# Performance work log

Measured on AMD Instinct MI355X. Metric: run time of the kernel, lower is better.

The kernel has to match this reference:

```python
import jax, jax.numpy as jnp
import numpy as np

D = 256      # d_model
H = 8        # num heads
HD = D // H  # head dim
DFF = 1024   # feedforward dim
S = 1024     # seq len
B = 8        # batch
EPS = 1e-5


def _layernorm(x, g, b):
    mu = jnp.mean(x, axis=-1, keepdims=True)
    var = jnp.mean((x - mu) ** 2, axis=-1, keepdims=True)
    return (x - mu) * jax.lax.rsqrt(var + EPS) * g + b


def setup_inputs() -> dict:
    key = jax.random.key(0)
    ks = jax.random.split(key, 12)
    xav = lambda k, shape: jax.random.uniform(
        k, shape, jnp.float32, -1.0, 1.0) * np.sqrt(6.0 / (shape[0] + shape[-1]))
    return {
        "src": jax.random.normal(ks[0], (S, B, D), jnp.float32),
        "bias": jax.random.normal(ks[1], (B, H, S, S), jnp.float32),
        "in_proj_w": xav(ks[2], (3 * D, D)),
        "in_proj_b": jnp.zeros((3 * D,), jnp.float32),
        "out_w": xav(ks[3], (D, D)),
        "out_b": jnp.zeros((D,), jnp.float32),
        "w1": xav(ks[4], (DFF, D)),
        "b1": jnp.zeros((DFF,), jnp.float32),
        "w2": xav(ks[5], (D, DFF)),
        "b2": jnp.zeros((D,), jnp.float32),
        "g1": jnp.ones((D,), jnp.float32),
        "be1": jnp.zeros((D,), jnp.float32),
        "g2": jnp.ones((D,), jnp.float32),
        "be2": jnp.zeros((D,), jnp.float32),
    }


def reference(src, bias, in_proj_w, in_proj_b, out_w, out_b,
              w1, b1, w2, b2, g1, be1, g2, be2):
    # Pre-norm (note: residual uses the NORMED src, matching the torch code)
    x = _layernorm(src, g1, be1)                       # [S,B,D]
    qkv = x @ in_proj_w.T + in_proj_b                  # [S,B,3D]
    q, k, v = jnp.split(qkv, 3, axis=-1)
    q = q * (HD ** -0.5)
    # [S,B,D] -> [B,H,S,HD]
    to_heads = lambda t: t.reshape(S, B, H, HD).transpose(1, 2, 0, 3)
    qh, kh, vh = to_heads(q), to_heads(k), to_heads(v)
    scores = jnp.einsum('bhsd,bhtd->bhst', qh, kh) + bias
    attn = jax.nn.softmax(scores, axis=-1)             # [B,H,S,S]
    ctx = jnp.einsum('bhst,bhtd->bhsd', attn, vh)      # [B,H,S,HD]
    ctx = ctx.transpose(2, 0, 1, 3).reshape(S, B, D)
    attn_out = ctx @ out_w.T + out_b
    x = x + attn_out                                   # residual (eval: no dropout)
    y = _layernorm(x, g2, be2)
    ff = jax.nn.relu(y @ w1.T + b1) @ w2.T + b2
    return y + ff
```

## Files before the change

### kernel.cpp

```cpp
#include <hip/hip_runtime.h>
#include <hip/hip_bf16.h>
#include <cstdint>

typedef unsigned short u16;
typedef __attribute__((ext_vector_type(8))) short bf16x8;
typedef __attribute__((ext_vector_type(4))) float f32x4;

#define S_LEN 1024
#define BATCH 8
#define DMODEL 256
#define NHEAD 8
#define HDIM 32
#define DFF 1024
#define NROWS (S_LEN * BATCH)

static __device__ __forceinline__ u16 f2b(float f) {
    union { float f; unsigned u; } x{f};
    unsigned r = (x.u + 0x7fffu + ((x.u >> 16) & 1u)) >> 16;
    return (u16)r;
}

__global__ __launch_bounds__(256) void convert_weights(
    const float* __restrict__ ipw, const float* __restrict__ outw,
    const float* __restrict__ w1, const float* __restrict__ w2,
    const float* __restrict__ ipb,
    u16* __restrict__ wqkv, u16* __restrict__ wout,
    u16* __restrict__ w1b, u16* __restrict__ w2b, float* __restrict__ bq)
{
    const float s = 0.17677669529663689f;
    const int i4 = (blockIdx.x * 256 + threadIdx.x) * 4;
    const float* src; u16* dst; int off; float sc = 1.0f;
    if (i4 < 196608)      { src = ipw;  dst = wqkv; off = 0;      if (i4 < 65536) sc = s; }
    else if (i4 < 262144) { src = outw; dst = wout; off = 196608; }
    else if (i4 < 524288) { src = w1;   dst = w1b;  off = 262144; }
    else                  { src = w2;   dst = w2b;  off = 524288; }
    const float4 v = *(const float4*)(src + i4 - off);
    uint2 pk;
    pk.x = (unsigned)f2b(v.x * sc) | ((unsigned)f2b(v.y * sc) << 16);
    pk.y = (unsigned)f2b(v.z * sc) | ((unsigned)f2b(v.w * sc) << 16);
    *(uint2*)(dst + i4 - off) = pk;
    if (i4 < 768) {
        const float4 b = *(const float4*)(ipb + i4);
        const float bs = (i4 < 256) ? s : 1.0f;
        *(float4*)(bq + i4) = make_float4(b.x * bs, b.y * bs, b.z * bs, b.w * bs);
    }
}

__global__ __launch_bounds__(256) void ln_kernel(
    const float* __restrict__ in, const float* __restrict__ g,
    const float* __restrict__ be, float* __restrict__ of, u16* __restrict__ ob)
{
    const int w = threadIdx.x >> 6, l = threadIdx.x & 63;
    const int row = blockIdx.x * 4 + w;
    const float4 v = *(const float4*)(in + (size_t)row * DMODEL + l * 4);
    float s = v.x + v.y + v.z + v.w;
    #pragma unroll
    for (int o = 32; o; o >>= 1) s += __shfl_xor(s, o);
    const float mu = s * (1.0f / DMODEL);
    const float dx = v.x - mu, dy = v.y - mu, dz = v.z - mu, dw = v.w - mu;
    float sq = dx * dx + dy * dy + dz * dz + dw * dw;
    #pragma unroll
    for (int o = 32; o; o >>= 1) sq += __shfl_xor(sq, o);
    const float rs = rsqrtf(sq * (1.0f / DMODEL) + 1e-5f);
    const float4 gv = *(const float4*)(g + l * 4);
    const float4 bv = *(const float4*)(be + l * 4);
    const float r0 = dx * rs * gv.x + bv.x;
    const float r1 = dy * rs * gv.y + bv.y;
    const float r2 = dz * rs * gv.z + bv.z;
    const float r3 = dw * rs * gv.w + bv.w;
    *(float4*)(of + (size_t)row * DMODEL + l * 4) = make_float4(r0, r1, r2, r3);
    uint2 pk;
    pk.x = (unsigned)f2b(r0) | ((unsigned)f2b(r1) << 16);
    pk.y = (unsigned)f2b(r2) | ((unsigned)f2b(r3) << 16);
    *(uint2*)(ob + (size_t)row * DMODEL + l * 4) = pk;
}

__global__ __launch_bounds__(256) void gemm_qkv(
    const u16* __restrict__ A, const u16* __restrict__ Bw,
    const float* __restrict__ bias,
    u16* __restrict__ Qh, u16* __restrict__ Kh, u16* __restrict__ Vt)
{
    __shared__ u16 sB[64 * 64];
    const int K = 256;
    const int tid = threadIdx.x, w = tid >> 6, l = tid & 63;
    const int g = l >> 4, q = l & 15;
    const int row = blockIdx.x * 64 + w * 16 + q;
    const int nbase = blockIdx.y * 64;
    f32x4 acc[4] = {{0,0,0,0},{0,0,0,0},{0,0,0,0},{0,0,0,0}};
    const u16* Arow = A + (size_t)row * K + g * 8;

    for (int kk = 0; kk < K; kk += 64) {
        __syncthreads();
        #pragma unroll
        for (int it = 0; it < 2; ++it) {
            const int idx = it * 256 + tid;
            const int br = idx >> 3, seg = idx & 7;
            const uint4 v = *(const uint4*)(Bw + (size_t)(nbase + br) * K + kk + seg * 8);
            *(uint4*)(&sB[(br * 128 + ((seg * 16) ^ ((br & 7) << 4))) >> 1]) = v;
        }
        __syncthreads();
        #pragma unroll
        for (int ks = 0; ks < 2; ++ks) {
            const bf16x8 af = *(const bf16x8*)(Arow + kk + ks * 32);
            #pragma unroll
            for (int n = 0; n < 4; ++n) {
                const int br = n * 16 + q;
                const bf16x8 bf = *(const bf16x8*)(
                    &sB[(br * 128 + ((ks * 64 + g * 16) ^ ((br & 7) << 4))) >> 1]);
                acc[n] = __builtin_amdgcn_mfma_f32_16x16x32_bf16(bf, af, acc[n], 0, 0, 0);
            }
        }
    }

    const int s = row >> 3, b = row & 7;
    if (nbase < 512) {
        u16* dst = (nbase >= 256) ? Kh : Qh;
        #pragma unroll
        for (int n = 0; n < 4; ++n) {
            const int col = nbase + n * 16 + g * 4;
            const float4 bv = *(const float4*)(bias + col);
            const int cc = col & 255, h = cc >> 5, hd = cc & 31;
            const int bh = b * 8 + h;
            uint2 pk;
            pk.x = (unsigned)f2b(acc[n][0] + bv.x) | ((unsigned)f2b(acc[n][1] + bv.y) << 16);
            pk.y = (unsigned)f2b(acc[n][2] + bv.z) | ((unsigned)f2b(acc[n][3] + bv.w) << 16);
            *(uint2*)(dst + ((size_t)bh * S_LEN + s) * HDIM + hd) = pk;
        }
    } else {
        #pragma unroll
        for (int n = 0; n < 4; ++n) {
            const int col = nbase + n * 16 + g * 4;
            const float4 bv = *(const float4*)(bias + col);
            const int cc = col - 512, h = cc >> 5, hd = cc & 31;
            const int bh = b * 8 + h;
            Vt[((size_t)bh * HDIM + hd + 0) * S_LEN + s] = f2b(acc[n][0] + bv.x);
            Vt[((size_t)bh * HDIM + hd + 1) * S_LEN + s] = f2b(acc[n][1] + bv.y);
            Vt[((size_t)bh * HDIM + hd + 2) * S_LEN + s] = f2b(acc[n][2] + bv.z);
            Vt[((size_t)bh * HDIM + hd + 3) * S_LEN + s] = f2b(acc[n][3] + bv.w);
        }
    }
}

__global__ __launch_bounds__(256) void attn_kernel(
    const u16* __restrict__ Qh, const u16* __restrict__ Kh,
    const u16* __restrict__ Vt, const float* __restrict__ bias,
    u16* __restrict__ ctx)
{
    __shared__ u16 sK[2][64 * 32];
    __shared__ u16 sV[2][32 * 64];
    __shared__ u16 sP[4][16 * 64];
    const int tid = threadIdx.x, w = tid >> 6, l = tid & 63;
    const int g = l >> 4, q = l & 15;
    const int bh = blockIdx.y, b = bh >> 3, h = bh & 7;
    const int qbase = blockIdx.x * 64 + w * 16;
    const int qrow = qbase + q;

    const bf16x8 qf = *(const bf16x8*)(Qh + ((size_t)bh * S_LEN + qrow) * HDIM + g * 8);
    const float* brow = bias + ((size_t)bh * S_LEN + qrow) * S_LEN;
    u16* Pw = sP[w];
    const int swz = (q & 7) << 4;

    const u16* KsrcBase = Kh + ((size_t)bh * S_LEN + w * 16 + q) * HDIM + g * 8;
    const u16* VsrcBase = Vt + ((size_t)bh * HDIM + (w & 1) * 16 + q) * S_LEN
                             + (w >> 1) * 32 + g * 8;
    u16* KdstA = &sK[0][tid * 8]; u16* KdstB = &sK[1][tid * 8];
    u16* VdstA = &sV[0][tid * 8]; u16* VdstB = &sV[1][tid * 8];

    f32x4 ctxa[2] = {{0,0,0,0},{0,0,0,0}};
    float m = -1e30f, lsum = 0.f;

    auto loadB = [&](int kt, f32x4* bv) {
        #pragma unroll
        for (int n = 0; n < 4; ++n)
            bv[n] = __builtin_nontemporal_load(
                (const f32x4*)(brow + kt * 64 + n * 16 + g * 4));
    };

    auto proc = [&](int buf, const f32x4* bv) {
        f32x4 sc[4];
        #pragma unroll
        for (int n = 0; n < 4; ++n) {
            const bf16x8 kf = *(const bf16x8*)(&sK[buf][(n * 64 + l) * 8]);
            f32x4 z = {0, 0, 0, 0};
            sc[n] = __builtin_amdgcn_mfma_f32_16x16x32_bf16(kf, qf, z, 0, 0, 0);
        }
        #pragma unroll
        for (int n = 0; n < 4; ++n)
            #pragma unroll
            for (int r = 0; r < 4; ++r) sc[n][r] += bv[n][r];

        float mx = sc[0][0];
        #pragma unroll
        for (int n = 0; n < 4; ++n)
            #pragma unroll
            for (int r = 0; r < 4; ++r) mx = fmaxf(mx, sc[n][r]);
        mx = fmaxf(mx, __shfl_xor(mx, 16));
        mx = fmaxf(mx, __shfl_xor(mx, 32));
        const float mn = fmaxf(m, mx);
        const float corr = __expf(m - mn);
        float su = 0.f;
        u16 pb[16];
        #pragma unroll
        for (int n = 0; n < 4; ++n)
            #pragma unroll
            for (int r = 0; r < 4; ++r) {
                const float pv = __expf(sc[n][r] - mn);
                su += pv;
                pb[n * 4 + r] = f2b(pv);
            }
        su += __shfl_xor(su, 16);
        su += __shfl_xor(su, 32);
        lsum = lsum * corr + su;
        m = mn;
        #pragma unroll
        for (int jg = 0; jg < 2; ++jg)
            #pragma unroll
            for (int r = 0; r < 4; ++r) ctxa[jg][r] *= corr;

        #pragma unroll
        for (int n = 0; n < 4; ++n) {
            uint2 pk;
            pk.x = (unsigned)pb[n * 4] | ((unsigned)pb[n * 4 + 1] << 16);
            pk.y = (unsigned)pb[n * 4 + 2] | ((unsigned)pb[n * 4 + 3] << 16);
            *(uint2*)((char*)Pw + q * 128 + ((n * 32 + g * 8) ^ swz)) = pk;
        }

        #pragma unroll
        for (int ks = 0; ks < 2; ++ks) {
            const bf16x8 pf = *(const bf16x8*)((char*)Pw + q * 128 + ((ks * 64 + g * 16) ^ swz));
            #pragma unroll
            for (int jg = 0; jg < 2; ++jg) {
                const bf16x8 vf = *(const bf16x8*)(&sV[buf][((ks * 2 + jg) * 64 + l) * 8]);
                ctxa[jg] = __builtin_amdgcn_mfma_f32_16x16x32_bf16(vf, pf, ctxa[jg], 0, 0, 0);
            }
        }
    };

    f32x4 bv0[4], bv1[4];
    {
        const uint4 kr = *(const uint4*)(KsrcBase);
        const uint4 vr = *(const uint4*)(VsrcBase);
        *(uint4*)KdstA = kr;
        *(uint4*)VdstA = vr;
        loadB(0, bv0);
    }
    __syncthreads();

    for (int kt = 0; kt < 16; kt += 2) {
        {
            uint4 kr, vr;
            kr = *(const uint4*)(KsrcBase + (size_t)(kt + 1) * 64 * HDIM);
            vr = *(const uint4*)(VsrcBase + (size_t)(kt + 1) * 64);
            loadB(kt + 1, bv1);
            proc(0, bv0);
            *(uint4*)KdstB = kr;
            *(uint4*)VdstB = vr;
        }
        __syncthreads();
        {
            uint4 kr, vr;
            if (kt + 2 < 16) {
                kr = *(const uint4*)(KsrcBase + (size_t)(kt + 2) * 64 * HDIM);
                vr = *(const uint4*)(VsrcBase + (size_t)(kt + 2) * 64);
                loadB(kt + 2, bv0);
            }
            proc(1, bv1);
            if (kt + 2 < 16) {
                *(uint4*)KdstA = kr;
                *(uint4*)VdstA = vr;
            }
        }
        __syncthreads();
    }

    const float inv = 1.0f / lsum;
    #pragma unroll
    for (int jg = 0; jg < 2; ++jg) {
        uint2 pk;
        pk.x = (unsigned)f2b(ctxa[jg][0] * inv) | ((unsigned)f2b(ctxa[jg][1] * inv) << 16);
        pk.y = (unsigned)f2b(ctxa[jg][2] * inv) | ((unsigned)f2b(ctxa[jg][3] * inv) << 16);
        *(uint2*)(ctx + ((size_t)qrow * 8 + b) * DMODEL + h * 32 + jg * 16 + g * 4) = pk;
    }
}

template <int MODE>
__global__ __launch_bounds__(256) void gemm_nt(
    const u16* __restrict__ A, const u16* __restrict__ Bw,
    const float* __restrict__ bias, const float* __restrict__ resid,
    float* __restrict__ outf, u16* __restrict__ outb,
    int N, int K)
{
    __shared__ u16 sB[64 * 64];
    const int tid = threadIdx.x, w = tid >> 6, l = tid & 63;
    const int g = l >> 4, q = l & 15;
    const int row = blockIdx.x * 64 + w * 16 + q;
    const int nbase = blockIdx.y * 64;
    f32x4 acc[4] = {{0,0,0,0},{0,0,0,0},{0,0,0,0},{0,0,0,0}};
    const u16* Arow = A + (size_t)row * K + g * 8;

    for (int kk = 0; kk < K; kk += 64) {
        __syncthreads();
        #pragma unroll
        for (int it = 0; it < 2; ++it) {
            const int idx = it * 256 + tid;
            const int br = idx >> 3, seg = idx & 7;
            const uint4 v = *(const uint4*)(Bw + (size_t)(nbase + br) * K + kk + seg * 8);
            *(uint4*)(&sB[(br * 128 + ((seg * 16) ^ ((br & 7) << 4))) >> 1]) = v;
        }
        __syncthreads();
        #pragma unroll
        for (int ks = 0; ks < 2; ++ks) {
            const bf16x8 af = *(const bf16x8*)(Arow + kk + ks * 32);
            #pragma unroll
            for (int n = 0; n < 4; ++n) {
                const int br = n * 16 + q;
                const bf16x8 bf = *(const bf16x8*)(
                    &sB[(br * 128 + ((ks * 64 + g * 16) ^ ((br & 7) << 4))) >> 1]);
                acc[n] = __builtin_amdgcn_mfma_f32_16x16x32_bf16(bf, af, acc[n], 0, 0, 0);
            }
        }
    }

    #pragma unroll
    for (int n = 0; n < 4; ++n) {
        const int col = nbase + n * 16 + g * 4;
        const float4 bv = *(const float4*)(bias + col);
        float v0 = acc[n][0] + bv.x, v1 = acc[n][1] + bv.y;
        float v2 = acc[n][2] + bv.z, v3 = acc[n][3] + bv.w;
        if (MODE == 2) {
            v0 = fmaxf(v0, 0.f); v1 = fmaxf(v1, 0.f);
            v2 = fmaxf(v2, 0.f); v3 = fmaxf(v3, 0.f);
            uint2 pk;
            pk.x = (unsigned)f2b(v0) | ((unsigned)f2b(v1) << 16);
            pk.y = (unsigned)f2b(v2) | ((unsigned)f2b(v3) << 16);
            *(uint2*)(outb + (size_t)row * N + col) = pk;
        } else {
            const float4 rv = *(const float4*)(resid + (size_t)row * N + col);
            *(float4*)(outf + (size_t)row * N + col) =
                make_float4(v0 + rv.x, v1 + rv.y, v2 + rv.z, v3 + rv.w);
        }
    }
}

__global__ __launch_bounds__(256) void oproj_ln(
    const u16* __restrict__ ctx, const u16* __restrict__ wob,
    const float* __restrict__ ob, const float* __restrict__ xf,
    const float* __restrict__ g2, const float* __restrict__ be2,
    float* __restrict__ yf, u16* __restrict__ yb)
{
    __shared__ float s1[4][16], s2[4][16];
    const int tid = threadIdx.x, wv = tid >> 6, l = tid & 63;
    const int g = l >> 4, q = l & 15;
    const int row = blockIdx.x * 16 + q;
    f32x4 acc[4] = {{0,0,0,0},{0,0,0,0},{0,0,0,0},{0,0,0,0}};
    const u16* Arow = ctx + (size_t)row * 256 + g * 8;
    const u16* Brow = wob + (size_t)(wv * 64 + q) * 256 + g * 8;

    #pragma unroll 2
    for (int kk = 0; kk < 256; kk += 32) {
        const bf16x8 af = *(const bf16x8*)(Arow + kk);
        #pragma unroll
        for (int n = 0; n < 4; ++n) {
            const bf16x8 bf = *(const bf16x8*)(Brow + (size_t)n * 16 * 256 + kk);
            acc[n] = __builtin_amdgcn_mfma_f32_16x16x32_bf16(bf, af, acc[n], 0, 0, 0);
        }
    }

    float sum = 0.f;
    #pragma unroll
    for (int n = 0; n < 4; ++n) {
        const int col = wv * 64 + n * 16 + g * 4;
        const float4 bv = *(const float4*)(ob + col);
        const float4 rv = *(const float4*)(xf + (size_t)row * 256 + col);
        acc[n][0] += bv.x + rv.x; acc[n][1] += bv.y + rv.y;
        acc[n][2] += bv.z + rv.z; acc[n][3] += bv.w + rv.w;
        sum += acc[n][0] + acc[n][1] + acc[n][2] + acc[n][3];
    }
    sum += __shfl_xor(sum, 16);
    sum += __shfl_xor(sum, 32);
    if (l < 16) s1[wv][q] = sum;
    __syncthreads();
    const float mu = (s1[0][q] + s1[1][q] + s1[2][q] + s1[3][q]) * (1.0f / 256);
    float sq = 0.f;
    #pragma unroll
    for (int n = 0; n < 4; ++n)
        #pragma unroll
        for (int r = 0; r < 4; ++r) {
            const float d = acc[n][r] - mu;
            sq += d * d;
        }
    sq += __shfl_xor(sq, 16);
    sq += __shfl_xor(sq, 32);
    if (l < 16) s2[wv][q] = sq;
    __syncthreads();
    const float rs = rsqrtf((s2[0][q] + s2[1][q] + s2[2][q] + s2[3][q]) * (1.0f / 256) + 1e-5f);

    #pragma unroll
    for (int n = 0; n < 4; ++n) {
        const int col = wv * 64 + n * 16 + g * 4;
        const float4 gv = *(const float4*)(g2 + col);
        const float4 b2 = *(const float4*)(be2 + col);
        const float y0 = (acc[n][0] - mu) * rs * gv.x + b2.x;
        const float y1 = (acc[n][1] - mu) * rs * gv.y + b2.y;
        const float y2 = (acc[n][2] - mu) * rs * gv.z + b2.z;
        const float y3 = (acc[n][3] - mu) * rs * gv.w + b2.w;
        *(float4*)(yf + (size_t)row * 256 + col) = make_float4(y0, y1, y2, y3);
        uint2 pk;
        pk.x = (unsigned)f2b(y0) | ((unsigned)f2b(y1) << 16);
        pk.y = (unsigned)f2b(y2) | ((unsigned)f2b(y3) << 16);
        *(uint2*)(yb + (size_t)row * 256 + col) = pk;
    }
}

extern "C" void kernel_launch(void* const* d_in, const int* in_sizes, int n_in,
                              void* d_out, int out_size, void* d_ws, size_t ws_size,
                              hipStream_t stream)
{
    const float* src  = (const float*)d_in[0];
    const float* bias = (const float*)d_in[1];
    const float* ipw  = (const float*)d_in[2];
    const float* ipb  = (const float*)d_in[3];
    const float* outw = (const float*)d_in[4];
    const float* outb = (const float*)d_in[5];
    const float* w1   = (const float*)d_in[6];
    const float* b1   = (const float*)d_in[7];
    const float* w2   = (const float*)d_in[8];
    const float* b2   = (const float*)d_in[9];
    const float* g1   = (const float*)d_in[10];
    const float* be1  = (const float*)d_in[11];
    const float* g2   = (const float*)d_in[12];
    const float* be2  = (const float*)d_in[13];

    char* p = (char*)d_ws;
    auto alloc = [&](size_t bytes) -> void* {
        void* r = (void*)p;
        p += (bytes + 255) & ~(size_t)255;
        return r;
    };
    float* xf   = (float*)alloc((size_t)NROWS * DMODEL * 4);
    u16*   xb   = (u16*)  alloc((size_t)NROWS * DMODEL * 2);
    u16*   Qh   = (u16*)  alloc((size_t)64 * S_LEN * HDIM * 2);
    u16*   Kb   = (u16*)  alloc((size_t)64 * S_LEN * HDIM * 2);
    u16*   Vt   = (u16*)  alloc((size_t)64 * S_LEN * HDIM * 2);
    u16*   ctx  = (u16*)  alloc((size_t)NROWS * DMODEL * 2);
    float* yf   = (float*)alloc((size_t)NROWS * DMODEL * 4);
    u16*   yb   = (u16*)  alloc((size_t)NROWS * DMODEL * 2);
    u16*   hb   = (u16*)  alloc((size_t)NROWS * DFF * 2);
    u16*   wqkv = (u16*)  alloc((size_t)768 * 256 * 2);
    u16*   wob  = (u16*)  alloc((size_t)256 * 256 * 2);
    u16*   w1b  = (u16*)  alloc((size_t)1024 * 256 * 2);
    u16*   w2b  = (u16*)  alloc((size_t)256 * 1024 * 2);
    float* bq   = (float*)alloc(768 * 4);

    convert_weights<<<768, 256, 0, stream>>>(ipw, outw, w1, w2, ipb, wqkv, wob, w1b, w2b, bq);
    ln_kernel<<<2048, 256, 0, stream>>>(src, g1, be1, xf, xb);
    gemm_qkv<<<dim3(128, 12), 256, 0, stream>>>(xb, wqkv, bq, Qh, Kb, Vt);
    attn_kernel<<<dim3(16, 64), 256, 0, stream>>>(Qh, Kb, Vt, bias, ctx);
    oproj_ln<<<512, 256, 0, stream>>>(ctx, wob, outb, xf, g2, be2, yf, yb);
    gemm_nt<2><<<dim3(128, 16), 256, 0, stream>>>(yb, w1b, b1, nullptr, nullptr, hb, 1024, 256);
    gemm_nt<3><<<dim3(128, 4), 256, 0, stream>>>(hb, w2b, b2, yf, (float*)d_out, nullptr, 256, 1024);
}
```

Before: 169.7 us.

## Merge weight conversion with LayerNorm and double-buffer GEMM B tiles

```diff
diff --git a/kernel.cpp b/kernel.cpp
--- a/kernel.cpp
+++ b/kernel.cpp
@@ -20,7 +20,9 @@
     return (u16)r;
 }
 
-__global__ __launch_bounds__(256) void convert_weights(
+__global__ __launch_bounds__(256) void prep_kernel(
+    const float* __restrict__ in, const float* __restrict__ g1,
+    const float* __restrict__ be1, float* __restrict__ of, u16* __restrict__ ob,
     const float* __restrict__ ipw, const float* __restrict__ outw,
     const float* __restrict__ w1, const float* __restrict__ w2,
     const float* __restrict__ ipb,
@@ -28,42 +30,39 @@
     u16* __restrict__ w1b, u16* __restrict__ w2b, float* __restrict__ bq)
 {
     const float s = 0.17677669529663689f;
-    const int i4 = (blockIdx.x * 256 + threadIdx.x) * 4;
-    const float* src; u16* dst; int off; float sc = 1.0f;
-    if (i4 < 196608)      { src = ipw;  dst = wqkv; off = 0;      if (i4 < 65536) sc = s; }
-    else if (i4 < 262144) { src = outw; dst = wout; off = 196608; }
-    else if (i4 < 524288) { src = w1;   dst = w1b;  off = 262144; }
-    else                  { src = w2;   dst = w2b;  off = 524288; }
-    const float4 v = *(const float4*)(src + i4 - off);
-    uint2 pk;
-    pk.x = (unsigned)f2b(v.x * sc) | ((unsigned)f2b(v.y * sc) << 16);
-    pk.y = (unsigned)f2b(v.z * sc) | ((unsigned)f2b(v.w * sc) << 16);
-    *(uint2*)(dst + i4 - off) = pk;
-    if (i4 < 768) {
-        const float4 b = *(const float4*)(ipb + i4);
-        const float bs = (i4 < 256) ? s : 1.0f;
-        *(float4*)(bq + i4) = make_float4(b.x * bs, b.y * bs, b.z * bs, b.w * bs);
-    }
-}
-
-__global__ __launch_bounds__(256) void ln_kernel(
-    const float* __restrict__ in, const float* __restrict__ g,
-    const float* __restrict__ be, float* __restrict__ of, u16* __restrict__ ob)
-{
+    if (blockIdx.x >= 2048) {
+        const int i4 = ((int)blockIdx.x - 2048) * 1024 + threadIdx.x * 4;
+        const float* src; u16* dst; int off; float sc = 1.0f;
+        if (i4 < 196608)      { src = ipw;  dst = wqkv; off = 0;      if (i4 < 65536) sc = s; }
+        else if (i4 < 262144) { src = outw; dst = wout; off = 196608; }
+        else if (i4 < 524288) { src = w1;   dst = w1b;  off = 262144; }
+        else                  { src = w2;   dst = w2b;  off = 524288; }
+        const float4 v = *(const float4*)(src + i4 - off);
+        uint2 pk;
+        pk.x = (unsigned)f2b(v.x * sc) | ((unsigned)f2b(v.y * sc) << 16);
+        pk.y = (unsigned)f2b(v.z * sc) | ((unsigned)f2b(v.w * sc) << 16);
+        *(uint2*)(dst + i4 - off) = pk;
+        if (i4 < 768) {
+            const float4 b = *(const float4*)(ipb + i4);
+            const float bs = (i4 < 256) ? s : 1.0f;
+            *(float4*)(bq + i4) = make_float4(b.x * bs, b.y * bs, b.z * bs, b.w * bs);
+        }
+        return;
+    }
     const int w = threadIdx.x >> 6, l = threadIdx.x & 63;
     const int row = blockIdx.x * 4 + w;
     const float4 v = *(const float4*)(in + (size_t)row * DMODEL + l * 4);
-    float s = v.x + v.y + v.z + v.w;
-    #pragma unroll
-    for (int o = 32; o; o >>= 1) s += __shfl_xor(s, o);
-    const float mu = s * (1.0f / DMODEL);
+    float s0 = v.x + v.y + v.z + v.w;
+    #pragma unroll
+    for (int o = 32; o; o >>= 1) s0 += __shfl_xor(s0, o);
+    const float mu = s0 * (1.0f / DMODEL);
     const float dx = v.x - mu, dy = v.y - mu, dz = v.z - mu, dw = v.w - mu;
     float sq = dx * dx + dy * dy + dz * dz + dw * dw;
     #pragma unroll
     for (int o = 32; o; o >>= 1) sq += __shfl_xor(sq, o);
     const float rs = rsqrtf(sq * (1.0f / DMODEL) + 1e-5f);
-    const float4 gv = *(const float4*)(g + l * 4);
-    const float4 bv = *(const float4*)(be + l * 4);
+    const float4 gv = *(const float4*)(g1 + l * 4);
+    const float4 bv = *(const float4*)(be1 + l * 4);
     const float r0 = dx * rs * gv.x + bv.x;
     const float r1 = dy * rs * gv.y + bv.y;
     const float r2 = dz * rs * gv.z + bv.z;
@@ -75,68 +74,141 @@
     *(uint2*)(ob + (size_t)row * DMODEL + l * 4) = pk;
 }
 
+template <int MF>
+__device__ __forceinline__ void gemm_core(
+    const u16* __restrict__ A, const u16* __restrict__ Bw,
+    int N, int K, int nbase, int rowbase, u16* sB, f32x4 acc[MF][4])
+{
+    const int tid = threadIdx.x, w = tid >> 6, l = tid & 63;
+    const int g = l >> 4, q = l & 15;
+    const u16* Arow = A + (size_t)(rowbase + w * (MF * 16) + q) * K + g * 8;
+
+    const int sbr = tid >> 3, sseg = tid & 7;
+    const size_t bsrc0 = (size_t)(nbase + sbr) * K + sseg * 8;
+    const size_t bsrc1 = (size_t)(nbase + sbr + 32) * K + sseg * 8;
+    const int d0 = sbr * 128 + ((sseg * 16) ^ ((sbr & 7) << 4));
+    const int d1 = d0 + 32 * 128;
+
+    {
+        const uint4 r0 = *(const uint4*)(Bw + bsrc0);
+        const uint4 r1 = *(const uint4*)(Bw + bsrc1);
+        *(uint4*)((char*)sB + d0) = r0;
+        *(uint4*)((char*)sB + d1) = r1;
+    }
+    const int NC = K >> 6;
+    for (int c = 0; c < NC; ++c) {
+        __syncthreads();
+        char* sBc = (char*)sB + (c & 1) * 8192;
+        char* sBn = (char*)sB + ((c + 1) & 1) * 8192;
+        uint4 p0, p1;
+        if (c + 1 < NC) {
+            p0 = *(const uint4*)(Bw + bsrc0 + (c + 1) * 64);
+            p1 = *(const uint4*)(Bw + bsrc1 + (c + 1) * 64);
+        }
+        const int kk = c * 64;
+        #pragma unroll
+        for (int ks = 0; ks < 2; ++ks) {
+            bf16x8 af[MF];
+            #pragma unroll
+            for (int m = 0; m < MF; ++m)
+                af[m] = *(const bf16x8*)(Arow + (size_t)m * 16 * K + kk + ks * 32);
+            #pragma unroll
+            for (int n = 0; n < 4; ++n) {
+                const int rr = n * 16 + q;
+                const bf16x8 bf = *(const bf16x8*)(
+                    sBc + rr * 128 + ((ks * 64 + g * 16) ^ ((rr & 7) << 4)));
+                #pragma unroll
+                for (int m = 0; m < MF; ++m)
+                    acc[m][n] = __builtin_amdgcn_mfma_f32_16x16x32_bf16(bf, af[m], acc[m][n], 0, 0, 0);
+            }
+        }
+        if (c + 1 < NC) {
+            *(uint4*)(sBn + d0) = p0;
+            *(uint4*)(sBn + d1) = p1;
+        }
+    }
+}
+
 __global__ __launch_bounds__(256) void gemm_qkv(
     const u16* __restrict__ A, const u16* __restrict__ Bw,
     const float* __restrict__ bias,
     u16* __restrict__ Qh, u16* __restrict__ Kh, u16* __restrict__ Vt)
 {
-    __shared__ u16 sB[64 * 64];
-    const int K = 256;
+    __shared__ u16 sB[2][64 * 64];
     const int tid = threadIdx.x, w = tid >> 6, l = tid & 63;
     const int g = l >> 4, q = l & 15;
-    const int row = blockIdx.x * 64 + w * 16 + q;
-    const int nbase = blockIdx.y * 64;
-    f32x4 acc[4] = {{0,0,0,0},{0,0,0,0},{0,0,0,0},{0,0,0,0}};
-    const u16* Arow = A + (size_t)row * K + g * 8;
-
-    for (int kk = 0; kk < K; kk += 64) {
-        __syncthreads();
-        #pragma unroll
-        for (int it = 0; it < 2; ++it) {
-            const int idx = it * 256 + tid;
-            const int br = idx >> 3, seg = idx & 7;
-            const uint4 v = *(const uint4*)(Bw + (size_t)(nbase + br) * K + kk + seg * 8);
-            *(uint4*)(&sB[(br * 128 + ((seg * 16) ^ ((br & 7) << 4))) >> 1]) = v;
-        }
-        __syncthreads();
-        #pragma unroll
-        for (int ks = 0; ks < 2; ++ks) {
-            const bf16x8 af = *(const bf16x8*)(Arow + kk + ks * 32);
+    const int rowbase = blockIdx.x * 128, nbase = blockIdx.y * 64;
+    f32x4 acc[2][4] = {};
+    gemm_core<2>(A, Bw, 768, 256, nbase, rowbase, &sB[0][0], acc);
+
+    #pragma unroll
+    for (int m = 0; m < 2; ++m) {
+        const int row = rowbase + w * 32 + m * 16 + q;
+        const int s = row >> 3, b = row & 7;
+        if (nbase < 512) {
+            u16* dst = (nbase >= 256) ? Kh : Qh;
             #pragma unroll
             for (int n = 0; n < 4; ++n) {
-                const int br = n * 16 + q;
-                const bf16x8 bf = *(const bf16x8*)(
-                    &sB[(br * 128 + ((ks * 64 + g * 16) ^ ((br & 7) << 4))) >> 1]);
-                acc[n] = __builtin_amdgcn_mfma_f32_16x16x32_bf16(bf, af, acc[n], 0, 0, 0);
-            }
-        }
-    }
-
-    const int s = row >> 3, b = row & 7;
-    if (nbase < 512) {
-        u16* dst = (nbase >= 256) ? Kh : Qh;
+                const int col = nbase + n * 16 + g * 4;
+                const float4 bv = *(const float4*)(bias + col);
+                const int cc = col & 255, h = cc >> 5, hd = cc & 31;
+                const int bh = b * 8 + h;
+                uint2 pk;
+                pk.x = (unsigned)f2b(acc[m][n][0] + bv.x) | ((unsigned)f2b(acc[m][n][1] + bv.y) << 16);
+                pk.y = (unsigned)f2b(acc[m][n][2] + bv.z) | ((unsigned)f2b(acc[m][n][3] + bv.w) << 16);
+                *(uint2*)(dst + ((size_t)bh * S_LEN + s) * HDIM + hd) = pk;
+            }
+        } else {
+            #pragma unroll
+            for (int n = 0; n < 4; ++n) {
+                const int col = nbase + n * 16 + g * 4;
+                const float4 bv = *(const float4*)(bias + col);
+                const int cc = col - 512, h = cc >> 5, hd = cc & 31;
+                const int bh = b * 8 + h;
+                Vt[((size_t)bh * HDIM + hd + 0) * S_LEN + s] = f2b(acc[m][n][0] + bv.x);
+                Vt[((size_t)bh * HDIM + hd + 1) * S_LEN + s] = f2b(acc[m][n][1] + bv.y);
+                Vt[((size_t)bh * HDIM + hd + 2) * S_LEN + s] = f2b(acc[m][n][2] + bv.z);
+                Vt[((size_t)bh * HDIM + hd + 3) * S_LEN + s] = f2b(acc[m][n][3] + bv.w);
+            }
+        }
+    }
+}
+
+template <int MODE, int MF>
+__global__ __launch_bounds__(256) void gemm_nt(
+    const u16* __restrict__ A, const u16* __restrict__ Bw,
+    const float* __restrict__ bias, const float* __restrict__ resid,
+    float* __restrict__ outf, u16* __restrict__ outb,
+    int N, int K)
+{
+    __shared__ u16 sB[2][64 * 64];
+    const int tid = threadIdx.x, w = tid >> 6, l = tid & 63;
+    const int g = l >> 4, q = l & 15;
+    const int rowbase = blockIdx.x * (MF * 64), nbase = blockIdx.y * 64;
+    f32x4 acc[MF][4] = {};
+    gemm_core<MF>(A, Bw, N, K, nbase, rowbase, &sB[0][0], acc);
+
+    #pragma unroll
+    for (int m = 0; m < MF; ++m) {
+        const int row = rowbase + w * (MF * 16) + m * 16 + q;
         #pragma unroll
         for (int n = 0; n < 4; ++n) {
             const int col = nbase + n * 16 + g * 4;
             const float4 bv = *(const float4*)(bias + col);
-            const int cc = col & 255, h = cc >> 5, hd = cc & 31;
-            const int bh = b * 8 + h;
-            uint2 pk;
-            pk.x = (unsigned)f2b(acc[n][0] + bv.x) | ((unsigned)f2b(acc[n][1] + bv.y) << 16);
-            pk.y = (unsigned)f2b(acc[n][2] + bv.z) | ((unsigned)f2b(acc[n][3] + bv.w) << 16);
-            *(uint2*)(dst + ((size_t)bh * S_LEN + s) * HDIM + hd) = pk;
-        }
-    } else {
-        #pragma unroll
-        for (int n = 0; n < 4; ++n) {
-            const int col = nbase + n * 16 + g * 4;
-            const float4 bv = *(const float4*)(bias + col);
-            const int cc = col - 512, h = cc >> 5, hd = cc & 31;
-            const int bh = b * 8 + h;
-            Vt[((size_t)bh * HDIM + hd + 0) * S_LEN + s] = f2b(acc[n][0] + bv.x);
-            Vt[((size_t)bh * HDIM + hd + 1) * S_LEN + s] = f2b(acc[n][1] + bv.y);
-            Vt[((size_t)bh * HDIM + hd + 2) * S_LEN + s] = f2b(acc[n][2] + bv.z);
-            Vt[((size_t)bh * HDIM + hd + 3) * S_LEN + s] = f2b(acc[n][3] + bv.w);
+            float v0 = acc[m][n][0] + bv.x, v1 = acc[m][n][1] + bv.y;
+            float v2 = acc[m][n][2] + bv.z, v3 = acc[m][n][3] + bv.w;
+            if (MODE == 2) {
+                v0 = fmaxf(v0, 0.f); v1 = fmaxf(v1, 0.f);
+                v2 = fmaxf(v2, 0.f); v3 = fmaxf(v3, 0.f);
+                uint2 pk;
+                pk.x = (unsigned)f2b(v0) | ((unsigned)f2b(v1) << 16);
+                pk.y = (unsigned)f2b(v2) | ((unsigned)f2b(v3) << 16);
+                *(uint2*)(outb + (size_t)row * N + col) = pk;
+            } else {
+                const float4 rv = *(const float4*)(resid + (size_t)row * N + col);
+                *(float4*)(outf + (size_t)row * N + col) =
+                    make_float4(v0 + rv.x, v1 + rv.y, v2 + rv.z, v3 + rv.w);
+            }
         }
     }
 }
@@ -280,65 +352,6 @@
         pk.x = (unsigned)f2b(ctxa[jg][0] * inv) | ((unsigned)f2b(ctxa[jg][1] * inv) << 16);
         pk.y = (unsigned)f2b(ctxa[jg][2] * inv) | ((unsigned)f2b(ctxa[jg][3] * inv) << 16);
         *(uint2*)(ctx + ((size_t)qrow * 8 + b) * DMODEL + h * 32 + jg * 16 + g * 4) = pk;
-    }
-}
-
-template <int MODE>
-__global__ __launch_bounds__(256) void gemm_nt(
-    const u16* __restrict__ A, const u16* __restrict__ Bw,
-    const float* __restrict__ bias, const float* __restrict__ resid,
-    float* __restrict__ outf, u16* __restrict__ outb,
-    int N, int K)
-{
-    __shared__ u16 sB[64 * 64];
-    const int tid = threadIdx.x, w = tid >> 6, l = tid & 63;
-    const int g = l >> 4, q = l & 15;
-    const int row = blockIdx.x * 64 + w * 16 + q;
-    const int nbase = blockIdx.y * 64;
-    f32x4 acc[4] = {{0,0,0,0},{0,0,0,0},{0,0,0,0},{0,0,0,0}};
-    const u16* Arow = A + (size_t)row * K + g * 8;
-
-    for (int kk = 0; kk < K; kk += 64) {
-        __syncthreads();
-        #pragma unroll
-        for (int it = 0; it < 2; ++it) {
-            const int idx = it * 256 + tid;
-            const int br = idx >> 3, seg = idx & 7;
-            const uint4 v = *(const uint4*)(Bw + (size_t)(nbase + br) * K + kk + seg * 8);
-            *(uint4*)(&sB[(br * 128 + ((seg * 16) ^ ((br & 7) << 4))) >> 1]) = v;
-        }
-        __syncthreads();
-        #pragma unroll
-        for (int ks = 0; ks < 2; ++ks) {
-            const bf16x8 af = *(const bf16x8*)(Arow + kk + ks * 32);
-            #pragma unroll
-            for (int n = 0; n < 4; ++n) {
-                const int br = n * 16 + q;
-                const bf16x8 bf = *(const bf16x8*)(
-                    &sB[(br * 128 + ((ks * 64 + g * 16) ^ ((br & 7) << 4))) >> 1]);
-                acc[n] = __builtin_amdgcn_mfma_f32_16x16x32_bf16(bf, af, acc[n], 0, 0, 0);
-            }
-        }
-    }
-
-    #pragma unroll
-    for (int n = 0; n < 4; ++n) {
-        const int col = nbase + n * 16 + g * 4;
-        const float4 bv = *(const float4*)(bias + col);
-        float v0 = acc[n][0] + bv.x, v1 = acc[n][1] + bv.y;
-        float v2 = acc[n][2] + bv.z, v3 = acc[n][3] + bv.w;
-        if (MODE == 2) {
-            v0 = fmaxf(v0, 0.f); v1 = fmaxf(v1, 0.f);
-            v2 = fmaxf(v2, 0.f); v3 = fmaxf(v3, 0.f);
-            uint2 pk;
-            pk.x = (unsigned)f2b(v0) | ((unsigned)f2b(v1) << 16);
-            pk.y = (unsigned)f2b(v2) | ((unsigned)f2b(v3) << 16);
-            *(uint2*)(outb + (size_t)row * N + col) = pk;
-        } else {
-            const float4 rv = *(const float4*)(resid + (size_t)row * N + col);
-            *(float4*)(outf + (size_t)row * N + col) =
-                make_float4(v0 + rv.x, v1 + rv.y, v2 + rv.z, v3 + rv.w);
-        }
     }
 }
 
@@ -452,11 +465,12 @@
     u16*   w2b  = (u16*)  alloc((size_t)256 * 1024 * 2);
     float* bq   = (float*)alloc(768 * 4);
 
-    convert_weights<<<768, 256, 0, stream>>>(ipw, outw, w1, w2, ipb, wqkv, wob, w1b, w2b, bq);
-    ln_kernel<<<2048, 256, 0, stream>>>(src, g1, be1, xf, xb);
-    gemm_qkv<<<dim3(128, 12), 256, 0, stream>>>(xb, wqkv, bq, Qh, Kb, Vt);
+    prep_kernel<<<2816, 256, 0, stream>>>(src, g1, be1, xf, xb,
+                                          ipw, outw, w1, w2, ipb,
+                                          wqkv, wob, w1b, w2b, bq);
+    gemm_qkv<<<dim3(64, 12), 256, 0, stream>>>(xb, wqkv, bq, Qh, Kb, Vt);
     attn_kernel<<<dim3(16, 64), 256, 0, stream>>>(Qh, Kb, Vt, bias, ctx);
     oproj_ln<<<512, 256, 0, stream>>>(ctx, wob, outb, xf, g2, be2, yf, yb);
-    gemm_nt<2><<<dim3(128, 16), 256, 0, stream>>>(yb, w1b, b1, nullptr, nullptr, hb, 1024, 256);
-    gemm_nt<3><<<dim3(128, 4), 256, 0, stream>>>(hb, w2b, b2, yf, (float*)d_out, nullptr, 256, 1024);
-}
+    gemm_nt<2, 2><<<dim3(64, 16), 256, 0, stream>>>(yb, w1b, b1, nullptr, nullptr, hb, 1024, 256);
+    gemm_nt<3, 1><<<dim3(128, 4), 256, 0, stream>>>(hb, w2b, b2, yf, (float*)d_out, nullptr, 256, 1024);
+}
```

Result: faster. 157.3 us (-7.3%).
